# Performance work log

Hardware: AMD Instinct MI355X
Metric: run time of the kernel (lower is better)

Reference implementation:

```python
import jax, jax.numpy as jnp
import numpy as np

N_NODES = 100000
N_EDGES = 1600000
N_GRAPHS = 512
NODE_DIM = 64   # len(node_indices)
GRAPH_DIM = 16  # len(graph_indices) == graph_channels
HIDDEN = 128
OUT = 8


def setup_inputs() -> dict:
    key = jax.random.key(0)
    ks = jax.random.split(key, 12)
    x = jax.random.normal(ks[0], (N_NODES, NODE_DIM + GRAPH_DIM), dtype=jnp.float32)
    edge_index = jax.random.randint(ks[1], (2, N_EDGES), 0, N_NODES, dtype=jnp.int64)
    batch = jnp.sort(jax.random.randint(ks[2], (N_NODES,), 0, N_GRAPHS, dtype=jnp.int64))
    def lin(k, fan_in, fan_out):
        lim = 1.0 / np.sqrt(fan_in)
        return jax.random.uniform(k, (fan_in, fan_out), jnp.float32, -lim, lim)
    return {
        "x": x, "edge_index": edge_index, "batch": batch,
        "W1": lin(ks[3], NODE_DIM, HIDDEN), "b1": jnp.zeros((HIDDEN,), jnp.float32),
        "W2": lin(ks[4], HIDDEN, HIDDEN),   "b2": jnp.zeros((HIDDEN,), jnp.float32),
        "Wm1": lin(ks[5], HIDDEN + GRAPH_DIM, HIDDEN), "bm1": jnp.zeros((HIDDEN,), jnp.float32),
        "Wm2": lin(ks[6], HIDDEN, OUT), "bm2": jnp.zeros((OUT,), jnp.float32),
    }


def _gcn_conv(h_in, src, dst, W, b):
    # PyG GCNConv: h = X W; out = D^{-1/2}(A+I)D^{-1/2} h + b, deg over A+I.
    h = h_in @ W                                        # [N, H]
    deg = jnp.zeros((N_NODES,), h.dtype).at[dst].add(1.0) + 1.0  # +1 self loop
    dinv = jax.lax.rsqrt(deg)                           # [N]
    norm = dinv[src] * dinv[dst]                        # [E]
    out = jnp.zeros_like(h).at[dst].add(norm[:, None] * h[src])
    out = out + (dinv * dinv)[:, None] * h              # self-loop term
    return out + b


def _mean_pool(v, batch):
    cnt = jax.ops.segment_sum(jnp.ones((v.shape[0],), v.dtype), batch, num_segments=N_GRAPHS)
    s = jax.ops.segment_sum(v, batch, num_segments=N_GRAPHS)
    return s / jnp.maximum(cnt, 1.0)[:, None]


def reference(x, edge_index, batch, W1, b1, W2, b2, Wm1, bm1, Wm2, bm2):
    src, dst = edge_index[0], edge_index[1]
    node_t = x[:, :NODE_DIM]                 # node_indices slice
    graph_t = _mean_pool(x[:, NODE_DIM:], batch)  # graph_indices slice, pooled [G, 16]
    h = _gcn_conv(node_t, src, dst, W1, b1)
    h = jax.nn.relu(h)                       # dropout is identity in eval mode
    h = _gcn_conv(h, src, dst, W2, b2)
    g = _mean_pool(h, batch)                 # [G, H]
    g = jnp.concatenate([g, graph_t], axis=1)
    g = jax.nn.relu(g @ Wm1 + bm1)
    return g @ Wm2 + bm2                     # [G, OUT]
```

## Files before the change

kernel.cpp:

```cpp
#include <hip/hip_runtime.h>
#include <hip/hip_bf16.h>

#define N_NODES 100000
#define N_EDGES 1600000
#define N_GRAPHS 512
#define NODE_DIM 64
#define GRAPH_DIM 16
#define HIDDEN 128
#define OUT_DIM 8

#define NBUCKETS 391
#define BIN_CAP 8192
#define EPB 4096


__global__ __launch_bounds__(256) void k_binplace(const int* __restrict__ src,
                                                  const int* __restrict__ dst,
                                                  int* __restrict__ gcur,
                                                  unsigned* __restrict__ bin) {
    __shared__ int cnt[NBUCKETS];
    __shared__ int base[NBUCKETS];
    int t = threadIdx.x;
    for (int i = t; i < NBUCKETS; i += 256) cnt[i] = 0;
    __syncthreads();
    int e0 = blockIdx.x * EPB;
#pragma unroll
    for (int k = 0; k < EPB / 256; k++) {
        int e = e0 + k * 256 + t;
        if (e < N_EDGES) atomicAdd(&cnt[dst[e] >> 8], 1);
    }
    __syncthreads();
    for (int i = t; i < NBUCKETS; i += 256) {
        int c = cnt[i];
        base[i] = (c > 0) ? atomicAdd(&gcur[i], c) : 0;
        cnt[i] = 0;
    }
    __syncthreads();
#pragma unroll
    for (int k = 0; k < EPB / 256; k++) {
        int e = e0 + k * 256 + t;
        if (e < N_EDGES) {
            int d = dst[e];
            int b = d >> 8;
            int p = atomicAdd(&cnt[b], 1);
            bin[(size_t)b * BIN_CAP + base[b] + p] = ((unsigned)src[e] << 8) | (unsigned)(d & 255);
        }
    }
}


__global__ __launch_bounds__(256) void k_degBf(const int* __restrict__ gcur,
                                               const unsigned* __restrict__ bin,
                                               int* __restrict__ degcnt,
                                               float* __restrict__ dinv,
                                               int* __restrict__ bsum) {
    __shared__ int cnt[256];
    int b = blockIdx.x, t = threadIdx.x;
    cnt[t] = 0;
    __syncthreads();
    int n = gcur[b];
    const unsigned* seg = bin + (size_t)b * BIN_CAP;
    for (int i = t; i < n; i += 256) atomicAdd(&cnt[seg[i] & 255u], 1);
    __syncthreads();
    int c = cnt[t];
    int node = b * 256 + t;
    if (node < N_NODES) {
        degcnt[node] = c;
        dinv[node] = rsqrtf((float)c + 1.0f);
    }
    __syncthreads();
    for (int o = 128; o > 0; o >>= 1) {
        if (t < o) cnt[t] += cnt[t + o];
        __syncthreads();
    }
    if (t == 0) bsum[b] = cnt[0];
}


__global__ __launch_bounds__(512) void k_scanb(const int* __restrict__ bsum,
                                               int* __restrict__ bofs) {
    __shared__ int s[512];
    int t = threadIdx.x;
    int v = (t < NBUCKETS) ? bsum[t] : 0;
    s[t] = v;
    __syncthreads();
    for (int o = 1; o < 512; o <<= 1) {
        int u = (t >= o) ? s[t - o] : 0;
        __syncthreads();
        s[t] += u;
        __syncthreads();
    }
    if (t < NBUCKETS) bofs[t] = s[t] - v;
}


__global__ __launch_bounds__(256) void k_rowfill(const int* __restrict__ degcnt,
                                                 const int* __restrict__ bofs,
                                                 const int* __restrict__ gcur,
                                                 const unsigned* __restrict__ bin,
                                                 const float* __restrict__ dinv,
                                                 int* __restrict__ row_start,
                                                 int* __restrict__ csr,
                                                 float* __restrict__ csrw) {
    __shared__ int sc[256];
    __shared__ int rsl[256];
    __shared__ int cnt[256];
    __shared__ float dl[256];
    int b = blockIdx.x, t = threadIdx.x;
    int node = b * 256 + t;
    int v = (node < N_NODES) ? degcnt[node] : 0;
    sc[t] = v;
    __syncthreads();
    for (int o = 1; o < 256; o <<= 1) {
        int u = (t >= o) ? sc[t - o] : 0;
        __syncthreads();
        sc[t] += u;
        __syncthreads();
    }
    int rs = bofs[b] + sc[t] - v;
    if (node < N_NODES) row_start[node] = rs;
    rsl[t] = rs;
    cnt[t] = 0;
    dl[t] = rsqrtf((float)v + 1.0f);
    __syncthreads();
    int n = gcur[b];
    const unsigned* seg = bin + (size_t)b * BIN_CAP;
    for (int i = t; i < n; i += 256) {
        unsigned e = seg[i];
        int dlidx = (int)(e & 255u);
        int s = (int)(e >> 8);
        int pos = rsl[dlidx] + atomicAdd(&cnt[dlidx], 1);
        csr[pos] = s;
        csrw[pos] = dinv[s] * dl[dlidx];
    }
}


__global__ __launch_bounds__(256) void k_packstat(const float* __restrict__ x,
                                                  const int* __restrict__ batch,
                                                  ushort* __restrict__ xb,
                                                  float* __restrict__ gt_sum) {
    int t = threadIdx.x;
    int i0 = blockIdx.x * 64;
    for (int idx = t; idx < 64 * 32; idx += 256) {
        int node = i0 + (idx >> 5);
        if (node < N_NODES) {
            int c2 = idx & 31;
            float2 v = *(const float2*)&x[(size_t)node * 80 + c2 * 2];
            __hip_bfloat16 lo = __float2bfloat16(v.x);
            __hip_bfloat16 hi = __float2bfloat16(v.y);
            ushort2 pv = make_ushort2(*(ushort*)&lo, *(ushort*)&hi);
            ((ushort2*)xb)[(size_t)node * 32 + c2] = pv;
        }
    }
    int c = t & 15, sub = t >> 4;
    int iend = min(i0 + 64, N_NODES);
    float acc = 0.0f;
    int g = -1;
    for (int i = i0 + sub; i < iend; i += 16) {
        int bi = batch[i];
        if (bi != g) {
            if (g >= 0) atomicAdd(&gt_sum[g * GRAPH_DIM + c], acc);
            acc = 0.0f; g = bi;
        }
        acc += x[(size_t)i * 80 + NODE_DIM + c];
    }
    if (g >= 0) atomicAdd(&gt_sum[g * GRAPH_DIM + c], acc);
}


#define LDX(s_) __uint_as_float((unsigned)xb[(size_t)(s_)*64 + lane] << 16)

__global__ __launch_bounds__(256) void k_gather1(const int* __restrict__ csr,
                                                 const float* __restrict__ csrw,
                                                 const int* __restrict__ row_start,
                                                 const float* __restrict__ dinv,
                                                 const ushort* __restrict__ xb,
                                                 float* __restrict__ z) {
    int w = threadIdx.x >> 6, lane = threadIdx.x & 63;
    int nA = blockIdx.x * 8 + w * 2;
    int nB = nA + 1;
    int rsA = row_start[nA], reA = (nA == N_NODES - 1) ? N_EDGES : row_start[nA + 1];
    int rsB = row_start[nB], reB = (nB == N_NODES - 1) ? N_EDGES : row_start[nB + 1];
    float aA0 = 0.f, aA1 = 0.f, aA2 = 0.f, aA3 = 0.f;
    float aB0 = 0.f, aB1 = 0.f, aB2 = 0.f, aB3 = 0.f;
    int kA = rsA, kB = rsB;
    while (kA + 4 <= reA && kB + 4 <= reB) {
        int a0 = csr[kA], a1 = csr[kA + 1], a2 = csr[kA + 2], a3 = csr[kA + 3];
        int b0 = csr[kB], b1 = csr[kB + 1], b2 = csr[kB + 2], b3 = csr[kB + 3];
        float wa0 = csrw[kA], wa1 = csrw[kA + 1], wa2 = csrw[kA + 2], wa3 = csrw[kA + 3];
        float wb0 = csrw[kB], wb1 = csrw[kB + 1], wb2 = csrw[kB + 2], wb3 = csrw[kB + 3];
        float vA0 = LDX(a0), vA1 = LDX(a1), vA2 = LDX(a2), vA3 = LDX(a3);
        float vB0 = LDX(b0), vB1 = LDX(b1), vB2 = LDX(b2), vB3 = LDX(b3);
        aA0 += wa0 * vA0; aA1 += wa1 * vA1; aA2 += wa2 * vA2; aA3 += wa3 * vA3;
        aB0 += wb0 * vB0; aB1 += wb1 * vB1; aB2 += wb2 * vB2; aB3 += wb3 * vB3;
        kA += 4; kB += 4;
    }
    while (kA + 4 <= reA) {
        int a0 = csr[kA], a1 = csr[kA + 1], a2 = csr[kA + 2], a3 = csr[kA + 3];
        float wa0 = csrw[kA], wa1 = csrw[kA + 1], wa2 = csrw[kA + 2], wa3 = csrw[kA + 3];
        float vA0 = LDX(a0), vA1 = LDX(a1), vA2 = LDX(a2), vA3 = LDX(a3);
        aA0 += wa0 * vA0; aA1 += wa1 * vA1; aA2 += wa2 * vA2; aA3 += wa3 * vA3;
        kA += 4;
    }
    while (kB + 4 <= reB) {
        int b0 = csr[kB], b1 = csr[kB + 1], b2 = csr[kB + 2], b3 = csr[kB + 3];
        float wb0 = csrw[kB], wb1 = csrw[kB + 1], wb2 = csrw[kB + 2], wb3 = csrw[kB + 3];
        float vB0 = LDX(b0), vB1 = LDX(b1), vB2 = LDX(b2), vB3 = LDX(b3);
        aB0 += wb0 * vB0; aB1 += wb1 * vB1; aB2 += wb2 * vB2; aB3 += wb3 * vB3;
        kB += 4;
    }
    while (kA < reA && kB < reB) {
        int a0 = csr[kA]; int b0 = csr[kB];
        float wa0 = csrw[kA], wb0 = csrw[kB];
        aA0 += wa0 * LDX(a0); aB0 += wb0 * LDX(b0);
        kA++; kB++;
    }
    while (kA < reA) { int a0 = csr[kA]; aA0 += csrw[kA] * LDX(a0); kA++; }
    while (kB < reB) { int b0 = csr[kB]; aB0 += csrw[kB] * LDX(b0); kB++; }
    float dA = dinv[nA], dB = dinv[nB];
    z[(size_t)nA * 64 + lane] = aA0 + aA1 + aA2 + aA3 + dA * dA * LDX(nA);
    z[(size_t)nB * 64 + lane] = aB0 + aB1 + aB2 + aB3 + dB * dB * LDX(nB);
}


__global__ __launch_bounds__(128) void k_gemm64(const float* __restrict__ A,
                                                const float* __restrict__ W,
                                                const float* __restrict__ bias,
                                                ushort* __restrict__ C, int nrows) {
    const int TM = 8, K = 64;
    __shared__ float As[TM][K];
    int row0 = blockIdx.x * TM;
    int j = threadIdx.x;
    for (int idx = threadIdx.x; idx < TM * K; idx += 128) {
        int m = idx / K, k = idx % K;
        int r = row0 + m;
        As[m][k] = (r < nrows) ? A[(size_t)r * K + k] : 0.0f;
    }
    __syncthreads();
    float acc[TM];
#pragma unroll
    for (int m = 0; m < TM; m++) acc[m] = 0.0f;
    for (int k = 0; k < K; k++) {
        float w = W[k * 128 + j];
#pragma unroll
        for (int m = 0; m < TM; m++) acc[m] += As[m][k] * w;
    }
    float b = bias[j];
#pragma unroll
    for (int m = 0; m < TM; m++) {
        int r = row0 + m;
        if (r < nrows) {
            float v = fmaxf(acc[m] + b, 0.0f);
            __hip_bfloat16 hv = __float2bfloat16(v);
            C[(size_t)r * 128 + j] = *(ushort*)&hv;
        }
    }
}


__global__ __launch_bounds__(256) void k_gather2(const int* __restrict__ csr,
                                                 const float* __restrict__ csrw,
                                                 const int* __restrict__ row_start,
                                                 const float* __restrict__ dinv,
                                                 const unsigned* __restrict__ h,
                                                 const int* __restrict__ batch,
                                                 float* __restrict__ gsum2) {
    __shared__ float2 red[8][64];
    int w = threadIdx.x >> 6, lane = threadIdx.x & 63;
    int nA = blockIdx.x * 8 + w * 2;
    int nB = nA + 1;
    int rsA = row_start[nA], reA = (nA == N_NODES - 1) ? N_EDGES : row_start[nA + 1];
    int rsB = row_start[nB], reB = (nB == N_NODES - 1) ? N_EDGES : row_start[nB + 1];
    float2 aA0 = {0.f,0.f}, aA1 = {0.f,0.f}, aA2 = {0.f,0.f}, aA3 = {0.f,0.f};
    float2 aB0 = {0.f,0.f}, aB1 = {0.f,0.f}, aB2 = {0.f,0.f}, aB3 = {0.f,0.f};
    int kA = rsA, kB = rsB;
#define FMA2(acc_, w_, u_) { acc_.x += (w_) * __uint_as_float((u_) << 16); \
                             acc_.y += (w_) * __uint_as_float((u_) & 0xffff0000u); }
    while (kA + 4 <= reA && kB + 4 <= reB) {
        int a0 = csr[kA], a1 = csr[kA + 1], a2 = csr[kA + 2], a3 = csr[kA + 3];
        int b0 = csr[kB], b1 = csr[kB + 1], b2 = csr[kB + 2], b3 = csr[kB + 3];
        float wa0 = csrw[kA], wa1 = csrw[kA + 1], wa2 = csrw[kA + 2], wa3 = csrw[kA + 3];
        float wb0 = csrw[kB], wb1 = csrw[kB + 1], wb2 = csrw[kB + 2], wb3 = csrw[kB + 3];
        unsigned uA0 = h[(size_t)a0 * 64 + lane], uA1 = h[(size_t)a1 * 64 + lane];
        unsigned uA2 = h[(size_t)a2 * 64 + lane], uA3 = h[(size_t)a3 * 64 + lane];
        unsigned uB0 = h[(size_t)b0 * 64 + lane], uB1 = h[(size_t)b1 * 64 + lane];
        unsigned uB2 = h[(size_t)b2 * 64 + lane], uB3 = h[(size_t)b3 * 64 + lane];
        FMA2(aA0, wa0, uA0); FMA2(aA1, wa1, uA1); FMA2(aA2, wa2, uA2); FMA2(aA3, wa3, uA3);
        FMA2(aB0, wb0, uB0); FMA2(aB1, wb1, uB1); FMA2(aB2, wb2, uB2); FMA2(aB3, wb3, uB3);
        kA += 4; kB += 4;
    }
    while (kA + 4 <= reA) {
        int a0 = csr[kA], a1 = csr[kA + 1], a2 = csr[kA + 2], a3 = csr[kA + 3];
        float wa0 = csrw[kA], wa1 = csrw[kA + 1], wa2 = csrw[kA + 2], wa3 = csrw[kA + 3];
        unsigned uA0 = h[(size_t)a0 * 64 + lane], uA1 = h[(size_t)a1 * 64 + lane];
        unsigned uA2 = h[(size_t)a2 * 64 + lane], uA3 = h[(size_t)a3 * 64 + lane];
        FMA2(aA0, wa0, uA0); FMA2(aA1, wa1, uA1); FMA2(aA2, wa2, uA2); FMA2(aA3, wa3, uA3);
        kA += 4;
    }
    while (kB + 4 <= reB) {
        int b0 = csr[kB], b1 = csr[kB + 1], b2 = csr[kB + 2], b3 = csr[kB + 3];
        float wb0 = csrw[kB], wb1 = csrw[kB + 1], wb2 = csrw[kB + 2], wb3 = csrw[kB + 3];
        unsigned uB0 = h[(size_t)b0 * 64 + lane], uB1 = h[(size_t)b1 * 64 + lane];
        unsigned uB2 = h[(size_t)b2 * 64 + lane], uB3 = h[(size_t)b3 * 64 + lane];
        FMA2(aB0, wb0, uB0); FMA2(aB1, wb1, uB1); FMA2(aB2, wb2, uB2); FMA2(aB3, wb3, uB3);
        kB += 4;
    }
    while (kA < reA && kB < reB) {
        int a0 = csr[kA]; int b0 = csr[kB];
        float wa0 = csrw[kA], wb0 = csrw[kB];
        unsigned uA0 = h[(size_t)a0 * 64 + lane], uB0 = h[(size_t)b0 * 64 + lane];
        FMA2(aA0, wa0, uA0); FMA2(aB0, wb0, uB0);
        kA++; kB++;
    }
    while (kA < reA) {
        int a0 = csr[kA]; float wa0 = csrw[kA];
        unsigned uA0 = h[(size_t)a0 * 64 + lane];
        FMA2(aA0, wa0, uA0); kA++;
    }
    while (kB < reB) {
        int b0 = csr[kB]; float wb0 = csrw[kB];
        unsigned uB0 = h[(size_t)b0 * 64 + lane];
        FMA2(aB0, wb0, uB0); kB++;
    }
    float dA = dinv[nA], dB = dinv[nB];
    unsigned usA = h[(size_t)nA * 64 + lane];
    unsigned usB = h[(size_t)nB * 64 + lane];
    float2 rA, rB;
    rA.x = aA0.x + aA1.x + aA2.x + aA3.x + dA * dA * __uint_as_float(usA << 16);
    rA.y = aA0.y + aA1.y + aA2.y + aA3.y + dA * dA * __uint_as_float(usA & 0xffff0000u);
    rB.x = aB0.x + aB1.x + aB2.x + aB3.x + dB * dB * __uint_as_float(usB << 16);
    rB.y = aB0.y + aB1.y + aB2.y + aB3.y + dB * dB * __uint_as_float(usB & 0xffff0000u);
    red[w * 2][lane] = rA;
    red[w * 2 + 1][lane] = rB;
    __syncthreads();
    int g0 = batch[blockIdx.x * 8];
    int g7 = batch[blockIdx.x * 8 + 7];
    if (g0 == g7) {
        if (w == 0) {
            float sx = 0.f, sy = 0.f;
#pragma unroll
            for (int q = 0; q < 8; q++) { sx += red[q][lane].x; sy += red[q][lane].y; }
            atomicAdd(&gsum2[g0 * 128 + 2 * lane], sx);
            atomicAdd(&gsum2[g0 * 128 + 2 * lane + 1], sy);
        }
    } else {
        int gA = batch[nA], gB = batch[nB];
        atomicAdd(&gsum2[gA * 128 + 2 * lane], rA.x);
        atomicAdd(&gsum2[gA * 128 + 2 * lane + 1], rA.y);
        atomicAdd(&gsum2[gB * 128 + 2 * lane], rB.x);
        atomicAdd(&gsum2[gB * 128 + 2 * lane + 1], rB.y);
    }
#undef FMA2
}


__global__ __launch_bounds__(128) void k_mlp(const float* __restrict__ gsum2,
                                             const float* __restrict__ gt_sum,
                                             const int* __restrict__ batch,
                                             const float* __restrict__ W2,
                                             const float* __restrict__ b2,
                                             const float* __restrict__ Wm1,
                                             const float* __restrict__ bm1,
                                             const float* __restrict__ Wm2,
                                             const float* __restrict__ bm2,
                                             float* __restrict__ out) {
    __shared__ float srow[HIDDEN];
    __shared__ float g144[HIDDEN + GRAPH_DIM];
    __shared__ float sm[HIDDEN];
    __shared__ int cnt_sh;
    int b = blockIdx.x;
    int j = threadIdx.x;
    float raw = gsum2[b * 128 + j];
    float gtraw = (j < GRAPH_DIM) ? gt_sum[b * GRAPH_DIM + j] : 0.0f;
    if (j == 0) {
        int lo = 0, hi = N_NODES;
        while (lo < hi) { int m = (lo + hi) >> 1; if (batch[m] < b) lo = m + 1; else hi = m; }
        int a = lo;
        lo = 0; hi = N_NODES;
        while (lo < hi) { int m = (lo + hi) >> 1; if (batch[m] < b + 1) lo = m + 1; else hi = m; }
        cnt_sh = lo - a;
    }
    __syncthreads();
    float inv = 1.0f / fmaxf((float)cnt_sh, 1.0f);
    srow[j] = raw * inv;
    if (j < GRAPH_DIM) g144[128 + j] = gtraw * inv;
    __syncthreads();
    float z = b2[j];
    for (int k = 0; k < 128; k++) z += srow[k] * W2[k * 128 + j];
    g144[j] = z;
    __syncthreads();
    float acc = bm1[j];
    for (int k = 0; k < HIDDEN + GRAPH_DIM; k++) acc += g144[k] * Wm1[k * 128 + j];
    sm[j] = fmaxf(acc, 0.0f);
    __syncthreads();
    if (j < OUT_DIM) {
        float o = bm2[j];
        for (int k = 0; k < 128; k++) o += sm[k] * Wm2[k * OUT_DIM + j];
        out[b * OUT_DIM + j] = o;
    }
}

extern "C" void kernel_launch(void* const* d_in, const int* in_sizes, int n_in,
                              void* d_out, int out_size, void* d_ws, size_t ws_size,
                              hipStream_t stream) {
    const float* x    = (const float*)d_in[0];
    const int*   edge = (const int*)d_in[1];
    const int*   src  = edge;
    const int*   dst  = edge + N_EDGES;
    const int*   batch= (const int*)d_in[2];
    const float* W1   = (const float*)d_in[3];
    const float* b1   = (const float*)d_in[4];
    const float* W2   = (const float*)d_in[5];
    const float* b2   = (const float*)d_in[6];
    const float* Wm1  = (const float*)d_in[7];
    const float* bm1  = (const float*)d_in[8];
    const float* Wm2  = (const float*)d_in[9];
    const float* bm2  = (const float*)d_in[10];
    float* out = (float*)d_out;

    char* ws = (char*)d_ws;
    char* p = ws;
    unsigned* bin   = (unsigned*)p;  p += (size_t)NBUCKETS * BIN_CAP * 4;
    float* A        = (float*)p;     p += (size_t)N_NODES * 64 * 4;
    ushort* h1b     = (ushort*)p;    p += (size_t)N_NODES * 128 * 2;
    ushort* xb      = (ushort*)p;    p += (size_t)N_NODES * 64 * 2;
    int*   csr      = (int*)p;       p += (size_t)N_EDGES * 4;
    float* csrw     = (float*)p;     p += (size_t)N_EDGES * 4;
    int*   degcnt   = (int*)p;       p += (size_t)NBUCKETS * 256 * 4;
    int*   row_start= (int*)p;       p += (size_t)N_NODES * 4;
    float* dinv     = (float*)p;     p += (size_t)N_NODES * 4;
    int*   gcur     = (int*)p;       p += (size_t)NBUCKETS * 4;
    int*   bsum     = (int*)p;       p += 512 * 4;
    int*   bofs     = (int*)p;       p += 512 * 4;
    float* gt_sum   = (float*)p;     p += (size_t)N_GRAPHS * GRAPH_DIM * 4;
    float* gsum2    = (float*)p;     p += (size_t)N_GRAPHS * 128 * 4;

    hipMemsetAsync(gcur,   0, (size_t)NBUCKETS * 4, stream);
    hipMemsetAsync(gt_sum, 0, (size_t)N_GRAPHS * GRAPH_DIM * 4, stream);
    hipMemsetAsync(gsum2,  0, (size_t)N_GRAPHS * 128 * 4, stream);

    k_binplace<<<(N_EDGES + EPB - 1) / EPB, 256, 0, stream>>>(src, dst, gcur, bin);
    k_degBf<<<NBUCKETS, 256, 0, stream>>>(gcur, bin, degcnt, dinv, bsum);
    k_scanb<<<1, 512, 0, stream>>>(bsum, bofs);
    k_rowfill<<<NBUCKETS, 256, 0, stream>>>(degcnt, bofs, gcur, bin, dinv, row_start, csr, csrw);

    k_packstat<<<(N_NODES + 63) / 64, 256, 0, stream>>>(x, batch, xb, gt_sum);

    k_gather1<<<N_NODES / 8, 256, 0, stream>>>(csr, csrw, row_start, dinv, xb, A);
    k_gemm64<<<(N_NODES + 7) / 8, 128, 0, stream>>>(A, W1, b1, h1b, N_NODES);

    k_gather2<<<N_NODES / 8, 256, 0, stream>>>(csr, csrw, row_start, dinv,
                                               (const unsigned*)h1b, batch, gsum2);

    k_mlp<<<N_GRAPHS, 128, 0, stream>>>(gsum2, gt_sum, batch, W2, b2, Wm1, bm1, Wm2, bm2, out);
}
```

Measured before the change: 267.9 us.

## Fuse layer-1 gather with GEMM, interleave CSR index/weight, fold memsets into kernels

Merges the first aggregation kernel with the 64x128 GEMM so each block keeps its 8 aggregated rows in shared memory and writes bf16 h1 directly. This removes the fp32 intermediate round trip and one launch. CSR column indices and weights are packed into an int2 array so each edge needs a single 8-byte load. Two memsets are replaced by zeroing inside earlier kernels, which relies on launch ordering and on the exact grid sizes to cover the buffers. In the fused kernel only half the threads do the GEMM, so that stage has less parallelism.

```diff
diff --git a/kernel.cpp b/kernel.cpp
--- a/kernel.cpp
+++ b/kernel.cpp
@@ -12,6 +12,9 @@
 #define NBUCKETS 391
 #define BIN_CAP 8192
 #define EPB 4096
+
+__device__ __forceinline__ float bflo(unsigned u) { return __uint_as_float(u << 16); }
+__device__ __forceinline__ float bfhi(unsigned u) { return __uint_as_float(u & 0xffff0000u); }
 
 
 __global__ __launch_bounds__(256) void k_binplace(const int* __restrict__ src,
@@ -100,13 +103,14 @@
                                                  const unsigned* __restrict__ bin,
                                                  const float* __restrict__ dinv,
                                                  int* __restrict__ row_start,
-                                                 int* __restrict__ csr,
-                                                 float* __restrict__ csrw) {
+                                                 int2* __restrict__ csre,
+                                                 float* __restrict__ gt_sum) {
     __shared__ int sc[256];
     __shared__ int rsl[256];
     __shared__ int cnt[256];
     __shared__ float dl[256];
     int b = blockIdx.x, t = threadIdx.x;
+    if (b < 32) gt_sum[b * 256 + t] = 0.0f;
     int node = b * 256 + t;
     int v = (node < N_NODES) ? degcnt[node] : 0;
     sc[t] = v;
@@ -130,8 +134,7 @@
         int dlidx = (int)(e & 255u);
         int s = (int)(e >> 8);
         int pos = rsl[dlidx] + atomicAdd(&cnt[dlidx], 1);
-        csr[pos] = s;
-        csrw[pos] = dinv[s] * dl[dlidx];
+        csre[pos] = make_int2(s, __float_as_int(dinv[s] * dl[dlidx]));
     }
 }
 
@@ -171,13 +174,18 @@
 
 #define LDX(s_) __uint_as_float((unsigned)xb[(size_t)(s_)*64 + lane] << 16)
 
-__global__ __launch_bounds__(256) void k_gather1(const int* __restrict__ csr,
-                                                 const float* __restrict__ csrw,
-                                                 const int* __restrict__ row_start,
-                                                 const float* __restrict__ dinv,
-                                                 const ushort* __restrict__ xb,
-                                                 float* __restrict__ z) {
-    int w = threadIdx.x >> 6, lane = threadIdx.x & 63;
+__global__ __launch_bounds__(256) void k_conv1(const int2* __restrict__ csre,
+                                               const int* __restrict__ row_start,
+                                               const float* __restrict__ dinv,
+                                               const ushort* __restrict__ xb,
+                                               const float* __restrict__ W,
+                                               const float* __restrict__ bias,
+                                               ushort* __restrict__ C,
+                                               float* __restrict__ gsum2) {
+    __shared__ float zs[8][64];
+    int t = threadIdx.x;
+    if (blockIdx.x < 256) gsum2[blockIdx.x * 256 + t] = 0.0f;
+    int w = t >> 6, lane = t & 63;
     int nA = blockIdx.x * 8 + w * 2;
     int nB = nA + 1;
     int rsA = row_start[nA], reA = (nA == N_NODES - 1) ? N_EDGES : row_start[nA + 1];
@@ -186,81 +194,65 @@
     float aB0 = 0.f, aB1 = 0.f, aB2 = 0.f, aB3 = 0.f;
     int kA = rsA, kB = rsB;
     while (kA + 4 <= reA && kB + 4 <= reB) {
-        int a0 = csr[kA], a1 = csr[kA + 1], a2 = csr[kA + 2], a3 = csr[kA + 3];
-        int b0 = csr[kB], b1 = csr[kB + 1], b2 = csr[kB + 2], b3 = csr[kB + 3];
-        float wa0 = csrw[kA], wa1 = csrw[kA + 1], wa2 = csrw[kA + 2], wa3 = csrw[kA + 3];
-        float wb0 = csrw[kB], wb1 = csrw[kB + 1], wb2 = csrw[kB + 2], wb3 = csrw[kB + 3];
-        float vA0 = LDX(a0), vA1 = LDX(a1), vA2 = LDX(a2), vA3 = LDX(a3);
-        float vB0 = LDX(b0), vB1 = LDX(b1), vB2 = LDX(b2), vB3 = LDX(b3);
-        aA0 += wa0 * vA0; aA1 += wa1 * vA1; aA2 += wa2 * vA2; aA3 += wa3 * vA3;
-        aB0 += wb0 * vB0; aB1 += wb1 * vB1; aB2 += wb2 * vB2; aB3 += wb3 * vB3;
+        int2 eA0 = csre[kA], eA1 = csre[kA + 1], eA2 = csre[kA + 2], eA3 = csre[kA + 3];
+        int2 eB0 = csre[kB], eB1 = csre[kB + 1], eB2 = csre[kB + 2], eB3 = csre[kB + 3];
+        float vA0 = LDX(eA0.x), vA1 = LDX(eA1.x), vA2 = LDX(eA2.x), vA3 = LDX(eA3.x);
+        float vB0 = LDX(eB0.x), vB1 = LDX(eB1.x), vB2 = LDX(eB2.x), vB3 = LDX(eB3.x);
+        aA0 += __int_as_float(eA0.y) * vA0; aA1 += __int_as_float(eA1.y) * vA1;
+        aA2 += __int_as_float(eA2.y) * vA2; aA3 += __int_as_float(eA3.y) * vA3;
+        aB0 += __int_as_float(eB0.y) * vB0; aB1 += __int_as_float(eB1.y) * vB1;
+        aB2 += __int_as_float(eB2.y) * vB2; aB3 += __int_as_float(eB3.y) * vB3;
         kA += 4; kB += 4;
     }
     while (kA + 4 <= reA) {
-        int a0 = csr[kA], a1 = csr[kA + 1], a2 = csr[kA + 2], a3 = csr[kA + 3];
-        float wa0 = csrw[kA], wa1 = csrw[kA + 1], wa2 = csrw[kA + 2], wa3 = csrw[kA + 3];
-        float vA0 = LDX(a0), vA1 = LDX(a1), vA2 = LDX(a2), vA3 = LDX(a3);
-        aA0 += wa0 * vA0; aA1 += wa1 * vA1; aA2 += wa2 * vA2; aA3 += wa3 * vA3;
+        int2 e0 = csre[kA], e1 = csre[kA + 1], e2 = csre[kA + 2], e3 = csre[kA + 3];
+        float v0 = LDX(e0.x), v1 = LDX(e1.x), v2 = LDX(e2.x), v3 = LDX(e3.x);
+        aA0 += __int_as_float(e0.y) * v0; aA1 += __int_as_float(e1.y) * v1;
+        aA2 += __int_as_float(e2.y) * v2; aA3 += __int_as_float(e3.y) * v3;
         kA += 4;
     }
     while (kB + 4 <= reB) {
-        int b0 = csr[kB], b1 = csr[kB + 1], b2 = csr[kB + 2], b3 = csr[kB + 3];
-        float wb0 = csrw[kB], wb1 = csrw[kB + 1], wb2 = csrw[kB + 2], wb3 = csrw[kB + 3];
-        float vB0 = LDX(b0), vB1 = LDX(b1), vB2 = LDX(b2), vB3 = LDX(b3);
-        aB0 += wb0 * vB0; aB1 += wb1 * vB1; aB2 += wb2 * vB2; aB3 += wb3 * vB3;
+        int2 e0 = csre[kB], e1 = csre[kB + 1], e2 = csre[kB + 2], e3 = csre[kB + 3];
+        float v0 = LDX(e0.x), v1 = LDX(e1.x), v2 = LDX(e2.x), v3 = LDX(e3.x);
+        aB0 += __int_as_float(e0.y) * v0; aB1 += __int_as_float(e1.y) * v1;
+        aB2 += __int_as_float(e2.y) * v2; aB3 += __int_as_float(e3.y) * v3;
         kB += 4;
     }
     while (kA < reA && kB < reB) {
-        int a0 = csr[kA]; int b0 = csr[kB];
-        float wa0 = csrw[kA], wb0 = csrw[kB];
-        aA0 += wa0 * LDX(a0); aB0 += wb0 * LDX(b0);
+        int2 eA = csre[kA]; int2 eB = csre[kB];
+        aA0 += __int_as_float(eA.y) * LDX(eA.x);
+        aB0 += __int_as_float(eB.y) * LDX(eB.x);
         kA++; kB++;
     }
-    while (kA < reA) { int a0 = csr[kA]; aA0 += csrw[kA] * LDX(a0); kA++; }
-    while (kB < reB) { int b0 = csr[kB]; aB0 += csrw[kB] * LDX(b0); kB++; }
+    while (kA < reA) { int2 e = csre[kA]; aA0 += __int_as_float(e.y) * LDX(e.x); kA++; }
+    while (kB < reB) { int2 e = csre[kB]; aB0 += __int_as_float(e.y) * LDX(e.x); kB++; }
     float dA = dinv[nA], dB = dinv[nB];
-    z[(size_t)nA * 64 + lane] = aA0 + aA1 + aA2 + aA3 + dA * dA * LDX(nA);
-    z[(size_t)nB * 64 + lane] = aB0 + aB1 + aB2 + aB3 + dB * dB * LDX(nB);
-}
-
-
-__global__ __launch_bounds__(128) void k_gemm64(const float* __restrict__ A,
-                                                const float* __restrict__ W,
-                                                const float* __restrict__ bias,
-                                                ushort* __restrict__ C, int nrows) {
-    const int TM = 8, K = 64;
-    __shared__ float As[TM][K];
-    int row0 = blockIdx.x * TM;
-    int j = threadIdx.x;
-    for (int idx = threadIdx.x; idx < TM * K; idx += 128) {
-        int m = idx / K, k = idx % K;
-        int r = row0 + m;
-        As[m][k] = (r < nrows) ? A[(size_t)r * K + k] : 0.0f;
-    }
-    __syncthreads();
-    float acc[TM];
-#pragma unroll
-    for (int m = 0; m < TM; m++) acc[m] = 0.0f;
-    for (int k = 0; k < K; k++) {
-        float w = W[k * 128 + j];
-#pragma unroll
-        for (int m = 0; m < TM; m++) acc[m] += As[m][k] * w;
-    }
-    float b = bias[j];
-#pragma unroll
-    for (int m = 0; m < TM; m++) {
-        int r = row0 + m;
-        if (r < nrows) {
+    zs[w * 2][lane]     = aA0 + aA1 + aA2 + aA3 + dA * dA * LDX(nA);
+    zs[w * 2 + 1][lane] = aB0 + aB1 + aB2 + aB3 + dB * dB * LDX(nB);
+    __syncthreads();
+    if (t < 128) {
+        int j = t;
+        float acc[8];
+#pragma unroll
+        for (int m = 0; m < 8; m++) acc[m] = 0.0f;
+        for (int k = 0; k < 64; k++) {
+            float wv = W[k * 128 + j];
+#pragma unroll
+            for (int m = 0; m < 8; m++) acc[m] += zs[m][k] * wv;
+        }
+        float b = bias[j];
+        size_t row0 = (size_t)blockIdx.x * 8;
+#pragma unroll
+        for (int m = 0; m < 8; m++) {
             float v = fmaxf(acc[m] + b, 0.0f);
             __hip_bfloat16 hv = __float2bfloat16(v);
-            C[(size_t)r * 128 + j] = *(ushort*)&hv;
-        }
-    }
-}
-
-
-__global__ __launch_bounds__(256) void k_gather2(const int* __restrict__ csr,
-                                                 const float* __restrict__ csrw,
+            C[(row0 + m) * 128 + j] = *(ushort*)&hv;
+        }
+    }
+}
+
+
+__global__ __launch_bounds__(256) void k_gather2(const int2* __restrict__ csre,
                                                  const int* __restrict__ row_start,
                                                  const float* __restrict__ dinv,
                                                  const unsigned* __restrict__ h,
@@ -275,62 +267,56 @@
     float2 aA0 = {0.f,0.f}, aA1 = {0.f,0.f}, aA2 = {0.f,0.f}, aA3 = {0.f,0.f};
     float2 aB0 = {0.f,0.f}, aB1 = {0.f,0.f}, aB2 = {0.f,0.f}, aB3 = {0.f,0.f};
     int kA = rsA, kB = rsB;
-#define FMA2(acc_, w_, u_) { acc_.x += (w_) * __uint_as_float((u_) << 16); \
-                             acc_.y += (w_) * __uint_as_float((u_) & 0xffff0000u); }
+#define FMA2(acc_, wbits_, u_) { float w_ = __int_as_float(wbits_); \
+                             acc_.x += w_ * bflo(u_); acc_.y += w_ * bfhi(u_); }
     while (kA + 4 <= reA && kB + 4 <= reB) {
-        int a0 = csr[kA], a1 = csr[kA + 1], a2 = csr[kA + 2], a3 = csr[kA + 3];
-        int b0 = csr[kB], b1 = csr[kB + 1], b2 = csr[kB + 2], b3 = csr[kB + 3];
-        float wa0 = csrw[kA], wa1 = csrw[kA + 1], wa2 = csrw[kA + 2], wa3 = csrw[kA + 3];
-        float wb0 = csrw[kB], wb1 = csrw[kB + 1], wb2 = csrw[kB + 2], wb3 = csrw[kB + 3];
-        unsigned uA0 = h[(size_t)a0 * 64 + lane], uA1 = h[(size_t)a1 * 64 + lane];
-        unsigned uA2 = h[(size_t)a2 * 64 + lane], uA3 = h[(size_t)a3 * 64 + lane];
-        unsigned uB0 = h[(size_t)b0 * 64 + lane], uB1 = h[(size_t)b1 * 64 + lane];
-        unsigned uB2 = h[(size_t)b2 * 64 + lane], uB3 = h[(size_t)b3 * 64 + lane];
-        FMA2(aA0, wa0, uA0); FMA2(aA1, wa1, uA1); FMA2(aA2, wa2, uA2); FMA2(aA3, wa3, uA3);
-        FMA2(aB0, wb0, uB0); FMA2(aB1, wb1, uB1); FMA2(aB2, wb2, uB2); FMA2(aB3, wb3, uB3);
+        int2 eA0 = csre[kA], eA1 = csre[kA + 1], eA2 = csre[kA + 2], eA3 = csre[kA + 3];
+        int2 eB0 = csre[kB], eB1 = csre[kB + 1], eB2 = csre[kB + 2], eB3 = csre[kB + 3];
+        unsigned uA0 = h[(size_t)eA0.x * 64 + lane], uA1 = h[(size_t)eA1.x * 64 + lane];
+        unsigned uA2 = h[(size_t)eA2.x * 64 + lane], uA3 = h[(size_t)eA3.x * 64 + lane];
+        unsigned uB0 = h[(size_t)eB0.x * 64 + lane], uB1 = h[(size_t)eB1.x * 64 + lane];
+        unsigned uB2 = h[(size_t)eB2.x * 64 + lane], uB3 = h[(size_t)eB3.x * 64 + lane];
+        FMA2(aA0, eA0.y, uA0); FMA2(aA1, eA1.y, uA1); FMA2(aA2, eA2.y, uA2); FMA2(aA3, eA3.y, uA3);
+        FMA2(aB0, eB0.y, uB0); FMA2(aB1, eB1.y, uB1); FMA2(aB2, eB2.y, uB2); FMA2(aB3, eB3.y, uB3);
         kA += 4; kB += 4;
     }
     while (kA + 4 <= reA) {
-        int a0 = csr[kA], a1 = csr[kA + 1], a2 = csr[kA + 2], a3 = csr[kA + 3];
-        float wa0 = csrw[kA], wa1 = csrw[kA + 1], wa2 = csrw[kA + 2], wa3 = csrw[kA + 3];
-        unsigned uA0 = h[(size_t)a0 * 64 + lane], uA1 = h[(size_t)a1 * 64 + lane];
-        unsigned uA2 = h[(size_t)a2 * 64 + lane], uA3 = h[(size_t)a3 * 64 + lane];
-        FMA2(aA0, wa0, uA0); FMA2(aA1, wa1, uA1); FMA2(aA2, wa2, uA2); FMA2(aA3, wa3, uA3);
+        int2 e0 = csre[kA], e1 = csre[kA + 1], e2 = csre[kA + 2], e3 = csre[kA + 3];
+        unsigned u0 = h[(size_t)e0.x * 64 + lane], u1 = h[(size_t)e1.x * 64 + lane];
+        unsigned u2 = h[(size_t)e2.x * 64 + lane], u3 = h[(size_t)e3.x * 64 + lane];
+        FMA2(aA0, e0.y, u0); FMA2(aA1, e1.y, u1); FMA2(aA2, e2.y, u2); FMA2(aA3, e3.y, u3);
         kA += 4;
     }
     while (kB + 4 <= reB) {
-        int b0 = csr[kB], b1 = csr[kB + 1], b2 = csr[kB + 2], b3 = csr[kB + 3];
-        float wb0 = csrw[kB], wb1 = csrw[kB + 1], wb2 = csrw[kB + 2], wb3 = csrw[kB + 3];
-        unsigned uB0 = h[(size_t)b0 * 64 + lane], uB1 = h[(size_t)b1 * 64 + lane];
-        unsigned uB2 = h[(size_t)b2 * 64 + lane], uB3 = h[(size_t)b3 * 64 + lane];
-        FMA2(aB0, wb0, uB0); FMA2(aB1, wb1, uB1); FMA2(aB2, wb2, uB2); FMA2(aB3, wb3, uB3);
+        int2 e0 = csre[kB], e1 = csre[kB + 1], e2 = csre[kB + 2], e3 = csre[kB + 3];
+        unsigned u0 = h[(size_t)e0.x * 64 + lane], u1 = h[(size_t)e1.x * 64 + lane];
+        unsigned u2 = h[(size_t)e2.x * 64 + lane], u3 = h[(size_t)e3.x * 64 + lane];
+        FMA2(aB0, e0.y, u0); FMA2(aB1, e1.y, u1); FMA2(aB2, e2.y, u2); FMA2(aB3, e3.y, u3);
         kB += 4;
     }
     while (kA < reA && kB < reB) {
-        int a0 = csr[kA]; int b0 = csr[kB];
-        float wa0 = csrw[kA], wb0 = csrw[kB];
-        unsigned uA0 = h[(size_t)a0 * 64 + lane], uB0 = h[(size_t)b0 * 64 + lane];
-        FMA2(aA0, wa0, uA0); FMA2(aB0, wb0, uB0);
+        int2 eA = csre[kA]; int2 eB = csre[kB];
+        unsigned uA = h[(size_t)eA.x * 64 + lane], uB = h[(size_t)eB.x * 64 + lane];
+        FMA2(aA0, eA.y, uA); FMA2(aB0, eB.y, uB);
         kA++; kB++;
     }
     while (kA < reA) {
-        int a0 = csr[kA]; float wa0 = csrw[kA];
-        unsigned uA0 = h[(size_t)a0 * 64 + lane];
-        FMA2(aA0, wa0, uA0); kA++;
+        int2 e = csre[kA]; unsigned u = h[(size_t)e.x * 64 + lane];
+        FMA2(aA0, e.y, u); kA++;
     }
     while (kB < reB) {
-        int b0 = csr[kB]; float wb0 = csrw[kB];
-        unsigned uB0 = h[(size_t)b0 * 64 + lane];
-        FMA2(aB0, wb0, uB0); kB++;
-    }
+        int2 e = csre[kB]; unsigned u = h[(size_t)e.x * 64 + lane];
+        FMA2(aB0, e.y, u); kB++;
+    }
+#undef FMA2
     float dA = dinv[nA], dB = dinv[nB];
     unsigned usA = h[(size_t)nA * 64 + lane];
     unsigned usB = h[(size_t)nB * 64 + lane];
     float2 rA, rB;
-    rA.x = aA0.x + aA1.x + aA2.x + aA3.x + dA * dA * __uint_as_float(usA << 16);
-    rA.y = aA0.y + aA1.y + aA2.y + aA3.y + dA * dA * __uint_as_float(usA & 0xffff0000u);
-    rB.x = aB0.x + aB1.x + aB2.x + aB3.x + dB * dB * __uint_as_float(usB << 16);
-    rB.y = aB0.y + aB1.y + aB2.y + aB3.y + dB * dB * __uint_as_float(usB & 0xffff0000u);
+    rA.x = aA0.x + aA1.x + aA2.x + aA3.x + dA * dA * bflo(usA);
+    rA.y = aA0.y + aA1.y + aA2.y + aA3.y + dA * dA * bfhi(usA);
+    rB.x = aB0.x + aB1.x + aB2.x + aB3.x + dB * dB * bflo(usB);
+    rB.y = aB0.y + aB1.y + aB2.y + aB3.y + dB * dB * bfhi(usB);
     red[w * 2][lane] = rA;
     red[w * 2 + 1][lane] = rB;
     __syncthreads();
@@ -351,7 +337,6 @@
         atomicAdd(&gsum2[gB * 128 + 2 * lane], rB.x);
         atomicAdd(&gsum2[gB * 128 + 2 * lane + 1], rB.y);
     }
-#undef FMA2
 }
 
 
@@ -422,11 +407,9 @@
     char* ws = (char*)d_ws;
     char* p = ws;
     unsigned* bin   = (unsigned*)p;  p += (size_t)NBUCKETS * BIN_CAP * 4;
-    float* A        = (float*)p;     p += (size_t)N_NODES * 64 * 4;
+    int2*  csre     = (int2*)p;      p += (size_t)N_EDGES * 8;
     ushort* h1b     = (ushort*)p;    p += (size_t)N_NODES * 128 * 2;
     ushort* xb      = (ushort*)p;    p += (size_t)N_NODES * 64 * 2;
-    int*   csr      = (int*)p;       p += (size_t)N_EDGES * 4;
-    float* csrw     = (float*)p;     p += (size_t)N_EDGES * 4;
     int*   degcnt   = (int*)p;       p += (size_t)NBUCKETS * 256 * 4;
     int*   row_start= (int*)p;       p += (size_t)N_NODES * 4;
     float* dinv     = (float*)p;     p += (size_t)N_NODES * 4;
@@ -436,21 +419,18 @@
     float* gt_sum   = (float*)p;     p += (size_t)N_GRAPHS * GRAPH_DIM * 4;
     float* gsum2    = (float*)p;     p += (size_t)N_GRAPHS * 128 * 4;
 
-    hipMemsetAsync(gcur,   0, (size_t)NBUCKETS * 4, stream);
-    hipMemsetAsync(gt_sum, 0, (size_t)N_GRAPHS * GRAPH_DIM * 4, stream);
-    hipMemsetAsync(gsum2,  0, (size_t)N_GRAPHS * 128 * 4, stream);
+    hipMemsetAsync(gcur, 0, (size_t)NBUCKETS * 4, stream);
 
     k_binplace<<<(N_EDGES + EPB - 1) / EPB, 256, 0, stream>>>(src, dst, gcur, bin);
     k_degBf<<<NBUCKETS, 256, 0, stream>>>(gcur, bin, degcnt, dinv, bsum);
     k_scanb<<<1, 512, 0, stream>>>(bsum, bofs);
-    k_rowfill<<<NBUCKETS, 256, 0, stream>>>(degcnt, bofs, gcur, bin, dinv, row_start, csr, csrw);
+    k_rowfill<<<NBUCKETS, 256, 0, stream>>>(degcnt, bofs, gcur, bin, dinv, row_start, csre, gt_sum);
 
     k_packstat<<<(N_NODES + 63) / 64, 256, 0, stream>>>(x, batch, xb, gt_sum);
 
-    k_gather1<<<N_NODES / 8, 256, 0, stream>>>(csr, csrw, row_start, dinv, xb, A);
-    k_gemm64<<<(N_NODES + 7) / 8, 128, 0, stream>>>(A, W1, b1, h1b, N_NODES);
-
-    k_gather2<<<N_NODES / 8, 256, 0, stream>>>(csr, csrw, row_start, dinv,
+    k_conv1<<<N_NODES / 8, 256, 0, stream>>>(csre, row_start, dinv, xb, W1, b1, h1b, gsum2);
+
+    k_gather2<<<N_NODES / 8, 256, 0, stream>>>(csre, row_start, dinv,
                                                (const unsigned*)h1b, batch, gsum2);
 
     k_mlp<<<N_GRAPHS, 128, 0, stream>>>(gsum2, gt_sum, batch, W2, b2, Wm1, bm1, Wm2, bm2, out);
```

Result: faster. 248.2 us (-7.3%).
